# Optimization experiments

Measured on AMD Instinct MI355X. Metric: run time of the kernel, lower is better.

The kernel has to match this reference:

```python
import jax, jax.numpy as jnp
import numpy as np

EMBED_DIMS = [8, 16, 8]      # prod = 1024 = embed_dim
HIDDEN_DIMS = [16, 16, 16]   # prod = 4096 = hidden_dim
RANK = 16
B, S = 4, 1024


def _make_cores(key, in_dims, out_dims, rank):
    d = len(in_dims)
    ranks = [1] + [rank] * (d - 1) + [1]
    cores = []
    for k in range(d):
        key, sub = jax.random.split(key)
        shape = (ranks[k], in_dims[k], out_dims[k], ranks[k + 1])
        scale = 1.0 / np.sqrt(in_dims[k] * ranks[k])
        cores.append((scale * jax.random.normal(sub, shape, dtype=jnp.float32)))
    return cores


def setup_inputs() -> dict:
    key = jax.random.key(0)
    k_x, k1, k2, kb1, kb2 = jax.random.split(key, 5)
    x = jax.random.normal(k_x, (B, S, 1024), dtype=jnp.float32)
    fc1 = _make_cores(k1, EMBED_DIMS, HIDDEN_DIMS, RANK)
    fc2 = _make_cores(k2, HIDDEN_DIMS, EMBED_DIMS, RANK)
    b1 = 0.01 * jax.random.normal(kb1, (4096,), dtype=jnp.float32)
    b2 = 0.01 * jax.random.normal(kb2, (1024,), dtype=jnp.float32)
    return {
        "x": x,
        "fc1_c0": fc1[0], "fc1_c1": fc1[1], "fc1_c2": fc1[2], "fc1_b": b1,
        "fc2_c0": fc2[0], "fc2_c1": fc2[1], "fc2_c2": fc2[2], "fc2_b": b2,
    }


def tt_linear(x_flat, cores, bias, in_dims):
    """TT-matrix x batch-of-vectors product. x_flat: [N, prod(in_dims)].

    Cores: core_k has shape [r_{k-1}, n_k, m_k, r_k] with r_0 = r_d = 1.
    Invariant: acc is [r_{k-1}, n_k, rest] with rest laid out as
    (n_{k+1}..n_d, N, m_1..m_{k-1}).
    """
    N = x_flat.shape[0]
    acc = x_flat.reshape((N,) + tuple(in_dims))      # [N, n1..nd]
    acc = jnp.moveaxis(acc, 0, -1)                   # [n1..nd, N]
    acc = acc.reshape(in_dims[0], -1)[None]          # [1, n1, rest]
    d = len(cores)
    for k, c in enumerate(cores):
        # contract previous rank + current input mode
        acc = jnp.einsum('pnR,pnmq->Rmq', acc, c)    # [rest, m_k, r_k]
        if k < d - 1:
            n_next = in_dims[k + 1]
            R, m, q = acc.shape
            acc = acc.reshape(n_next, R // n_next, m, q)
            acc = jnp.transpose(acc, (3, 0, 1, 2)).reshape(q, n_next, -1)
    # final acc: [N * m1..m_{d-1}, m_d, 1] -> [N, M]
    return acc.reshape(N, -1) + bias


def reference(x, fc1_c0, fc1_c1, fc1_c2, fc1_b, fc2_c0, fc2_c1, fc2_c2, fc2_b):
    flat = x.reshape(-1, x.shape[-1])                        # [N, embed_dim]
    z1 = tt_linear(flat, [fc1_c0, fc1_c1, fc1_c2], fc1_b, EMBED_DIMS)   # [N, hidden]
    h1 = jax.nn.gelu(z1, approximate=False)                  # exact erf GELU (torch default)
    z2 = tt_linear(h1, [fc2_c0, fc2_c1, fc2_c2], fc2_b, HIDDEN_DIMS)    # [N, embed]
    return z2.reshape(*x.shape[:-1], z2.shape[-1])
```

## Files before the change

### kernel.cpp

```cpp
#include <hip/hip_runtime.h>
#include <stdint.h>

__device__ __forceinline__ float b2f(unsigned short u) {
    union { uint32_t i; float f; } v; v.i = ((uint32_t)u) << 16; return v.f;
}
__device__ __forceinline__ unsigned short f2b(float f) {
    union { float f; uint32_t i; } v; v.f = f;
    uint32_t r = v.i + 0x7fffu + ((v.i >> 16) & 1u);
    return (unsigned short)(r >> 16);
}

typedef __bf16 bf16x8 __attribute__((ext_vector_type(8)));
typedef float  f32x16 __attribute__((ext_vector_type(16)));

template<int N3, int M3>
__device__ __forceinline__ void build_T_body(int e,
                                             const float* __restrict__ c1,
                                             const float* __restrict__ c2,
                                             float* __restrict__ T) {
    int m3 = e % M3;
    int t  = e / M3;
    int n3 = t % N3;
    int rm = t / N3;
    float s = 0.f;
#pragma unroll
    for (int r2 = 0; r2 < 16; ++r2)
        s += c1[rm * 16 + r2] * c2[(r2 * N3 + n3) * M3 + m3];
    T[e] = s;
}

__global__ __launch_bounds__(256)
void prep_stage1(const float* __restrict__ c11, const float* __restrict__ c12,
                 float* __restrict__ T1,
                 const float* __restrict__ c21, const float* __restrict__ c22,
                 float* __restrict__ T2,
                 const float* __restrict__ x, unsigned short* __restrict__ xb) {
    const int b = blockIdx.x;
    if (b < 2048) {
        build_T_body<8, 16>(b * 256 + threadIdx.x, c11, c12, T1);
    } else if (b < 4096) {
        build_T_body<16, 8>((b - 2048) * 256 + threadIdx.x, c21, c22, T2);
    } else {
        const int t = (b - 4096) * 256 + threadIdx.x;
        const float4* p = (const float4*)(x + (size_t)t * 8);
        float4 f0 = p[0], f1 = p[1];
        int4 o;
        o.x = (uint32_t)f2b(f0.x) | ((uint32_t)f2b(f0.y) << 16);
        o.y = (uint32_t)f2b(f0.z) | ((uint32_t)f2b(f0.w) << 16);
        o.z = (uint32_t)f2b(f1.x) | ((uint32_t)f2b(f1.y) << 16);
        o.w = (uint32_t)f2b(f1.z) | ((uint32_t)f2b(f1.w) << 16);
        ((int4*)xb)[t] = o;
    }
}

template<int N1, int N2, int N3, int M1, int M2, int M3>
__device__ __forceinline__ void build_W_body(int t,
                                             const float* __restrict__ c0,
                                             const float* __restrict__ T,
                                             unsigned short* __restrict__ W) {
    constexpr int K = N1 * N2 * N3;
    int m3 = t % M3;
    int m2 = (t / M3) % M2;
    int n2 = (t / (M3 * M2)) % N2;
    int m1 = (t / (M3 * M2 * N2)) % M1;
    int n1 =  t / (M3 * M2 * N2 * M1);

    float c0r[16];
    const float4* c0p = (const float4*)(c0 + (n1 * M1 + m1) * 16);
#pragma unroll
    for (int i = 0; i < 4; ++i) ((float4*)c0r)[i] = c0p[i];

    float acc[N3] = {};
#pragma unroll
    for (int r1 = 0; r1 < 16; ++r1) {
        const float* Tp = T + (size_t)(((r1 * 16 + n2) * 16 + m2) * N3) * M3 + m3;
#pragma unroll
        for (int n3 = 0; n3 < N3; ++n3)
            acc[n3] += c0r[r1] * Tp[n3 * M3];
    }

    unsigned short ob[N3];
#pragma unroll
    for (int n3 = 0; n3 < N3; ++n3) ob[n3] = f2b(acc[n3]);

    unsigned short* dst = W + (size_t)((m1 * M2 + m2) * M3 + m3) * K
                            + (n1 * N2 + n2) * N3;
#pragma unroll
    for (int c = 0; c < N3 / 8; ++c)
        ((int4*)dst)[c] = ((const int4*)ob)[c];
}

__global__ __launch_bounds__(256)
void build_W_both(const float* __restrict__ c10, const float* __restrict__ T1,
                  unsigned short* __restrict__ W1,
                  const float* __restrict__ c20, const float* __restrict__ T2,
                  unsigned short* __restrict__ W2) {
    const int b = blockIdx.x;
    if (b < 2048)
        build_W_body<8, 16, 8, 16, 16, 16>(b * 256 + threadIdx.x, c10, T1, W1);
    else
        build_W_body<16, 16, 16, 8, 16, 8>((b - 2048) * 256 + threadIdx.x, c20, T2, W2);
}

template<int N1, int N2, int N3, int M1, int M2, int M3>
__global__ __launch_bounds__(256)
void build_W(const float* __restrict__ c0, const float* __restrict__ T,
             unsigned short* __restrict__ W) {
    build_W_body<N1, N2, N3, M1, M2, M3>(blockIdx.x * 256 + threadIdx.x, c0, T, W);
}

template<int BM, int BN, int KTOT, int GX, bool DO_GELU, bool C_F32>
__global__ __launch_bounds__(256, 2)
void gemm_gl(const unsigned short* __restrict__ A,
             const unsigned short* __restrict__ Bt,
             const float* __restrict__ bias,
             void* __restrict__ Cv,
             int Ncols)
{
    constexpr int BK   = 64;
    constexpr int NT   = KTOT / BK;
    constexpr int ASZ  = BM * BK;
    constexpr int BSZ  = BN * BK;
    constexpr int BUFE = ASZ + BSZ;
    constexpr int ACH  = BM / 32;
    constexpr int BCH  = BN / 32;
    constexpr int FI   = BM / 64, FJ = BN / 64;

    extern __shared__ unsigned short sh[];

    const int tid   = threadIdx.x;
    const int lane  = tid & 63;
    const int wave  = tid >> 6;
    const int m32   = lane & 31;
    const int khalf = lane >> 5;
    const int waveM = (wave >> 1) * (BM / 2);
    const int waveN = (wave & 1) * (BN / 2);
    const int srow  = tid >> 3;
    const int sslot = tid & 7;

    int lin = (int)blockIdx.y * GX + (int)blockIdx.x;
    const int total = GX * (int)gridDim.y;
    lin = (lin & 7) * (total >> 3) + (lin >> 3);
    const int rowBase = (lin / GX) * BM;
    const int colBase = (lin % GX) * BN;

#define GL_STAGE(B_, K0_)                                                     \
    {                                                                         \
        _Pragma("unroll")                                                     \
        for (int c = 0; c < ACH; ++c) {                                       \
            const int r  = c * 32 + srow;                                     \
            const int jg = sslot ^ (r & 7) ^ ((r >> 3) & 7);                  \
            const unsigned short* src = A +                                   \
                (size_t)(rowBase + r) * KTOT + (K0_) + jg * 8;                \
            unsigned short* dst = sh + (B_) * BUFE + c * 2048 + wave * 512;   \
            __builtin_amdgcn_global_load_lds(                                 \
                (const __attribute__((address_space(1))) void*)src,           \
                (__attribute__((address_space(3))) void*)dst, 16, 0, 0);      \
        }                                                                     \
        _Pragma("unroll")                                                     \
        for (int c = 0; c < BCH; ++c) {                                       \
            const int r  = c * 32 + srow;                                     \
            const int jg = sslot ^ (r & 7) ^ ((r >> 3) & 7);                  \
            const unsigned short* src = Bt +                                  \
                (size_t)(colBase + r) * KTOT + (K0_) + jg * 8;                \
            unsigned short* dst = sh + (B_) * BUFE + ASZ + c * 2048           \
                                  + wave * 512;                               \
            __builtin_amdgcn_global_load_lds(                                 \
                (const __attribute__((address_space(1))) void*)src,           \
                (__attribute__((address_space(3))) void*)dst, 16, 0, 0);      \
        }                                                                     \
    }

    f32x16 acc[FI][FJ] = {};

    GL_STAGE(0, 0)
    __syncthreads();

    int buf = 0;
    for (int t = 0; t < NT; ++t) {
        if (t + 1 < NT) GL_STAGE(buf ^ 1, (t + 1) * BK)

        const unsigned short* Ab = sh + buf * BUFE;
        const unsigned short* Bb = Ab + ASZ;
#pragma unroll
        for (int ks = 0; ks < 4; ++ks) {
            bf16x8 a_f[FI], b_f[FJ];
            const int g = ks * 2 + khalf;
#pragma unroll
            for (int i = 0; i < FI; ++i) {
                const int r = waveM + i * 32 + m32;
                const int key = (r & 7) ^ ((r >> 3) & 7);
                a_f[i] = *(const bf16x8*)&Ab[r * BK + ((g ^ key) << 3)];
            }
#pragma unroll
            for (int j = 0; j < FJ; ++j) {
                const int r = waveN + j * 32 + m32;
                const int key = (r & 7) ^ ((r >> 3) & 7);
                b_f[j] = *(const bf16x8*)&Bb[r * BK + ((g ^ key) << 3)];
            }
#pragma unroll
            for (int i = 0; i < FI; ++i)
#pragma unroll
                for (int j = 0; j < FJ; ++j)
                    acc[i][j] = __builtin_amdgcn_mfma_f32_32x32x16_bf16(
                        a_f[i], b_f[j], acc[i][j], 0, 0, 0);
        }
        __syncthreads();
        buf ^= 1;
    }
#undef GL_STAGE

#pragma unroll
    for (int i = 0; i < FI; ++i) {
#pragma unroll
        for (int j = 0; j < FJ; ++j) {
            const int col = colBase + waveN + j * 32 + m32;
            const float bv = bias[col];
#pragma unroll
            for (int reg = 0; reg < 16; ++reg) {
                const int row = rowBase + waveM + i * 32 +
                                (reg & 3) + 8 * (reg >> 2) + 4 * khalf;
                float z = acc[i][j][reg] + bv;
                if (DO_GELU)
                    z = 0.5f * z * (1.f + erff(z * 0.70710678118654752f));
                const size_t off = (size_t)row * Ncols + col;
                if (C_F32) ((float*)Cv)[off] = z;
                else       ((unsigned short*)Cv)[off] = f2b(z);
            }
        }
    }
}

#define PC_COMPUTE(BUF)                                                       \
    {                                                                         \
        _Pragma("unroll")                                                     \
        for (int ks = 0; ks < 4; ++ks) {                                      \
            bf16x8 a_f[FI], b_f[FJ];                                          \
            _Pragma("unroll")                                                 \
            for (int i = 0; i < FI; ++i) {                                    \
                const int key = (m32 & 7) ^                                   \
                    (((waveM >> 3) + 4 * i + (m32 >> 3)) & 7);                \
                const int slot = ((ks * 2 + khalf) ^ key) * 8;                \
                a_f[i] = *(const bf16x8*)&As[(BUF) * ASZ +                    \
                          (waveM + i * 32 + m32) * BK + slot];                \
            }                                                                 \
            _Pragma("unroll")                                                 \
            for (int j = 0; j < FJ; ++j) {                                    \
                const int key = (m32 & 7) ^                                   \
                    (((waveN >> 3) + 4 * j + (m32 >> 3)) & 7);                \
                const int slot = ((ks * 2 + khalf) ^ key) * 8;                \
                b_f[j] = *(const bf16x8*)&Bs[(BUF) * BSZ +                    \
                          (waveN + j * 32 + m32) * BK + slot];                \
            }                                                                 \
            _Pragma("unroll")                                                 \
            for (int i = 0; i < FI; ++i)                                      \
                _Pragma("unroll")                                             \
                for (int j = 0; j < FJ; ++j)                                  \
                    acc[i][j] = __builtin_amdgcn_mfma_f32_32x32x16_bf16(      \
                        a_f[i], b_f[j], acc[i][j], 0, 0, 0);                  \
        }                                                                     \
    }

template<int BM, int BN, int KTOT, bool DO_GELU, bool A_F32, bool C_F32>
__global__ __launch_bounds__(512, 4)
void gemm_pc(const void* __restrict__ Av,
             const unsigned short* __restrict__ Bt,
             const float* __restrict__ bias,
             void* __restrict__ Cv,
             int Ncols) {
    constexpr int BK  = 64;
    constexpr int CA  = BM / 8;
    constexpr int CB  = BN / 8;
    constexpr int PA  = CA / 4;
    constexpr int PB  = CB / 4;
    constexpr int FI  = BM / 64;
    constexpr int FJ  = BN / 64;
    constexpr int ASZ = BM * BK;
    constexpr int BSZ = BN * BK;
    __shared__ unsigned short As[2 * ASZ];
    __shared__ unsigned short Bs[2 * BSZ];

    const int tid  = threadIdx.x;
    const int lane = tid & 63;
    const int wave = tid >> 6;
    const int rowBase = blockIdx.y * BM;
    const int colBase = blockIdx.x * BN;

    const int lr    = lane >> 3;
    const int jj    = lane & 7;
    const int m32   = lane & 31;
    const int khalf = lane >> 5;

    if (wave >= 4) {
        const int pw = wave - 4;
#pragma unroll
        for (int it = 0; it < PA; ++it) {
            const int c  = pw * PA + it;
            const int jg = jj ^ lr ^ (c & 7);
            const size_t aoff = (size_t)(rowBase + c * 8 + lr) * KTOT + jg * 8;
            int4 v;
            if (A_F32) {
                const float* ga = (const float*)Av + aoff;
                float4 f0 = *(const float4*)ga;
                float4 f1 = *(const float4*)(ga + 4);
                v.x = (uint32_t)f2b(f0.x) | ((uint32_t)f2b(f0.y) << 16);
                v.y = (uint32_t)f2b(f0.z) | ((uint32_t)f2b(f0.w) << 16);
                v.z = (uint32_t)f2b(f1.x) | ((uint32_t)f2b(f1.y) << 16);
                v.w = (uint32_t)f2b(f1.z) | ((uint32_t)f2b(f1.w) << 16);
            } else {
                v = *(const int4*)((const unsigned short*)Av + aoff);
            }
            *(int4*)&As[c * 512 + lane * 8] = v;
        }
#pragma unroll
        for (int it = 0; it < PB; ++it) {
            const int c  = pw * PB + it;
            const int jg = jj ^ lr ^ (c & 7);
            *(int4*)&Bs[c * 512 + lane * 8] =
                *(const int4*)(Bt + (size_t)(colBase + c * 8 + lr) * KTOT + jg * 8);
        }
        __syncthreads();

        int buf = 1;
        for (int k0 = BK; k0 < KTOT; k0 += BK) {
            int4 aR[PA], bR[PB];
#pragma unroll
            for (int it = 0; it < PA; ++it) {
                const int c  = pw * PA + it;
                const int jg = jj ^ lr ^ (c & 7);
                const size_t aoff = (size_t)(rowBase + c * 8 + lr) * KTOT + k0 + jg * 8;
                if (A_F32) {
                    const float* ga = (const float*)Av + aoff;
                    float4 f0 = *(const float4*)ga;
                    float4 f1 = *(const float4*)(ga + 4);
                    int4 v;
                    v.x = (uint32_t)f2b(f0.x) | ((uint32_t)f2b(f0.y) << 16);
                    v.y = (uint32_t)f2b(f0.z) | ((uint32_t)f2b(f0.w) << 16);
                    v.z = (uint32_t)f2b(f1.x) | ((uint32_t)f2b(f1.y) << 16);
                    v.w = (uint32_t)f2b(f1.z) | ((uint32_t)f2b(f1.w) << 16);
                    aR[it] = v;
                } else {
                    aR[it] = *(const int4*)((const unsigned short*)Av + aoff);
                }
            }
#pragma unroll
            for (int it = 0; it < PB; ++it) {
                const int c  = pw * PB + it;
                const int jg = jj ^ lr ^ (c & 7);
                bR[it] = *(const int4*)(Bt + (size_t)(colBase + c * 8 + lr) * KTOT + k0 + jg * 8);
            }
#pragma unroll
            for (int it = 0; it < PA; ++it) {
                const int c = pw * PA + it;
                *(int4*)&As[buf * ASZ + c * 512 + lane * 8] = aR[it];
            }
#pragma unroll
            for (int it = 0; it < PB; ++it) {
                const int c = pw * PB + it;
                *(int4*)&Bs[buf * BSZ + c * 512 + lane * 8] = bR[it];
            }
            __syncthreads();
            buf ^= 1;
        }
    } else {
        const int waveM = (wave >> 1) * (BM / 2);
        const int waveN = (wave & 1) * (BN / 2);
        f32x16 acc[FI][FJ] = {};

        __syncthreads();

        int cur = 0;
        for (int k0 = BK; k0 < KTOT; k0 += BK) {
            PC_COMPUTE(cur)
            __syncthreads();
            cur ^= 1;
        }
        PC_COMPUTE(cur)

#pragma unroll
        for (int i = 0; i < FI; ++i) {
#pragma unroll
            for (int j = 0; j < FJ; ++j) {
                const int col = colBase + waveN + j * 32 + m32;
                const float bv = bias[col];
#pragma unroll
                for (int reg = 0; reg < 16; ++reg) {
                    const int row = rowBase + waveM + i * 32 +
                                    (reg & 3) + 8 * (reg >> 2) + 4 * khalf;
                    float z = acc[i][j][reg] + bv;
                    if (DO_GELU)
                        z = 0.5f * z * (1.f + erff(z * 0.70710678118654752f));
                    const size_t off = (size_t)row * Ncols + col;
                    if (C_F32) ((float*)Cv)[off] = z;
                    else       ((unsigned short*)Cv)[off] = f2b(z);
                }
            }
        }
    }
}

extern "C" void kernel_launch(void* const* d_in, const int* in_sizes, int n_in,
                              void* d_out, int out_size, void* d_ws, size_t ws_size,
                              hipStream_t stream) {
    const float* x      = (const float*)d_in[0];
    const float* fc1_c0 = (const float*)d_in[1];
    const float* fc1_c1 = (const float*)d_in[2];
    const float* fc1_c2 = (const float*)d_in[3];
    const float* fc1_b  = (const float*)d_in[4];
    const float* fc2_c0 = (const float*)d_in[5];
    const float* fc2_c1 = (const float*)d_in[6];
    const float* fc2_c2 = (const float*)d_in[7];
    const float* fc2_b  = (const float*)d_in[8];

    float* T1 = (float*)d_out;
    float* T2 = (float*)d_out + 524288;
    unsigned short* xb = (unsigned short*)((char*)d_out + (4u << 20));

    char* ws = (char*)d_ws;
    const bool big = ws_size >= (48ull << 20);

    constexpr int LDS1 = 2 * (128 + 128) * 64 * 2;
    constexpr int LDS2 = 2 * (128 + 64) * 64 * 2;
    static bool attr_done = false;
    if (!attr_done) {
        attr_done = true;
        (void)hipFuncSetAttribute(
            reinterpret_cast<const void*>(
                &gemm_gl<128, 128, 1024, 32, true, false>),
            hipFuncAttributeMaxDynamicSharedMemorySize, LDS1);
        (void)hipFuncSetAttribute(
            reinterpret_cast<const void*>(
                &gemm_gl<128, 64, 4096, 16, false, true>),
            hipFuncAttributeMaxDynamicSharedMemorySize, LDS2);
    }

    prep_stage1<<<6144, 256, 0, stream>>>(fc1_c1, fc1_c2, T1,
                                          fc2_c1, fc2_c2, T2, x, xb);

    if (big) {
        unsigned short* W1 = (unsigned short*)ws;
        unsigned short* W2 = (unsigned short*)(ws + (8u << 20));
        unsigned short* h  = (unsigned short*)(ws + (16u << 20));

        build_W_both<<<3072, 256, 0, stream>>>(fc1_c0, T1, W1,
                                               fc2_c0, T2, W2);
        gemm_gl<128, 128, 1024, 32, true, false>
            <<<dim3(32, 32), 256, LDS1, stream>>>(xb, W1, fc1_b, h, 4096);
        gemm_gl<128, 64, 4096, 16, false, true>
            <<<dim3(16, 32), 256, LDS2, stream>>>(h, W2, fc2_b, d_out, 1024);
    } else {
        unsigned short* W = (unsigned short*)ws;
        unsigned short* h = (unsigned short*)(ws + (8u << 20));

        build_W<8, 16, 8, 16, 16, 16><<<2048, 256, 0, stream>>>(fc1_c0, T1, W);
        gemm_pc<128, 128, 1024, true, false, false>
            <<<dim3(32, 32), 512, 0, stream>>>(xb, W, fc1_b, h, 4096);
        build_W<16, 16, 16, 8, 16, 8><<<1024, 256, 0, stream>>>(fc2_c0, T2, W);
        gemm_pc<128, 64, 4096, false, false, true>
            <<<dim3(16, 32), 512, 0, stream>>>(h, W, fc2_b, d_out, 1024);
    }
}
```

Measured before the change: 219.2 us.

## Use split-K with atomic accumulation for second GEMM and shrink K tile

Replaces the GEMM kernel with a variant that uses a 32-wide K tile, a smaller LDS footprint and a 4-blocks-per-CU launch bound. The second GEMM is split into two K chunks across a z grid dimension, and partial sums are added with atomics into an output that a separate kernel pre-fills with the bias. The aim is more blocks in flight and better occupancy for the tall-K second GEMM. The cost is an extra bias-fill launch, atomic traffic, and non-deterministic float summation order.

```diff
diff --git a/kernel.cpp b/kernel.cpp
--- a/kernel.cpp
+++ b/kernel.cpp
@@ -109,21 +109,28 @@
     build_W_body<N1, N2, N3, M1, M2, M3>(blockIdx.x * 256 + threadIdx.x, c0, T, W);
 }
 
-template<int BM, int BN, int KTOT, int GX, bool DO_GELU, bool C_F32>
-__global__ __launch_bounds__(256, 2)
-void gemm_gl(const unsigned short* __restrict__ A,
-             const unsigned short* __restrict__ Bt,
-             const float* __restrict__ bias,
-             void* __restrict__ Cv,
-             int Ncols)
+__global__ __launch_bounds__(256)
+void bias_fill(const float* __restrict__ b, float4* __restrict__ out) {
+    int t = blockIdx.x * 256 + threadIdx.x;
+    out[t] = ((const float4*)b)[t & 255];
+}
+
+template<int BM, int BN, int KCH, int KSTR, int GX, int GY,
+         bool DO_GELU, bool ATOMIC>
+__global__ __launch_bounds__(256, 4)
+void gemm_gl2(const unsigned short* __restrict__ A,
+              const unsigned short* __restrict__ Bt,
+              const float* __restrict__ bias,
+              void* __restrict__ Cv,
+              int Ncols)
 {
-    constexpr int BK   = 64;
-    constexpr int NT   = KTOT / BK;
+    constexpr int BK   = 32;
+    constexpr int NT   = KCH / BK;
     constexpr int ASZ  = BM * BK;
     constexpr int BSZ  = BN * BK;
     constexpr int BUFE = ASZ + BSZ;
-    constexpr int ACH  = BM / 32;
-    constexpr int BCH  = BN / 32;
+    constexpr int ACH  = BM / 64;
+    constexpr int BCH  = BN / 64;
     constexpr int FI   = BM / 64, FJ = BN / 64;
 
     extern __shared__ unsigned short sh[];
@@ -135,23 +142,24 @@
     const int khalf = lane >> 5;
     const int waveM = (wave >> 1) * (BM / 2);
     const int waveN = (wave & 1) * (BN / 2);
-    const int srow  = tid >> 3;
-    const int sslot = tid & 7;
-
-    int lin = (int)blockIdx.y * GX + (int)blockIdx.x;
-    const int total = GX * (int)gridDim.y;
+    const int srow  = tid >> 2;
+    const int sslot = tid & 3;
+
+    int lin = ((int)blockIdx.z * GY + (int)blockIdx.y) * GX + (int)blockIdx.x;
+    const int total = GX * GY * (int)gridDim.z;
     lin = (lin & 7) * (total >> 3) + (lin >> 3);
-    const int rowBase = (lin / GX) * BM;
     const int colBase = (lin % GX) * BN;
-
-#define GL_STAGE(B_, K0_)                                                     \
+    const int rowBase = ((lin / GX) % GY) * BM;
+    const int kOff    = (lin / (GX * GY)) * KCH;
+
+#define GL2_STAGE(B_, K0_)                                                    \
     {                                                                         \
         _Pragma("unroll")                                                     \
         for (int c = 0; c < ACH; ++c) {                                       \
-            const int r  = c * 32 + srow;                                     \
-            const int jg = sslot ^ (r & 7) ^ ((r >> 3) & 7);                  \
+            const int r  = c * 64 + srow;                                     \
+            const int jg = sslot ^ (((r >> 1) & 3) ^ ((r >> 3) & 3));         \
             const unsigned short* src = A +                                   \
-                (size_t)(rowBase + r) * KTOT + (K0_) + jg * 8;                \
+                (size_t)(rowBase + r) * KSTR + (K0_) + jg * 8;                \
             unsigned short* dst = sh + (B_) * BUFE + c * 2048 + wave * 512;   \
             __builtin_amdgcn_global_load_lds(                                 \
                 (const __attribute__((address_space(1))) void*)src,           \
@@ -159,10 +167,10 @@
         }                                                                     \
         _Pragma("unroll")                                                     \
         for (int c = 0; c < BCH; ++c) {                                       \
-            const int r  = c * 32 + srow;                                     \
-            const int jg = sslot ^ (r & 7) ^ ((r >> 3) & 7);                  \
+            const int r  = c * 64 + srow;                                     \
+            const int jg = sslot ^ (((r >> 1) & 3) ^ ((r >> 3) & 3));         \
             const unsigned short* src = Bt +                                  \
-                (size_t)(colBase + r) * KTOT + (K0_) + jg * 8;                \
+                (size_t)(colBase + r) * KSTR + (K0_) + jg * 8;                \
             unsigned short* dst = sh + (B_) * BUFE + ASZ + c * 2048           \
                                   + wave * 512;                               \
             __builtin_amdgcn_global_load_lds(                                 \
@@ -173,29 +181,29 @@
 
     f32x16 acc[FI][FJ] = {};
 
-    GL_STAGE(0, 0)
+    GL2_STAGE(0, kOff)
     __syncthreads();
 
     int buf = 0;
     for (int t = 0; t < NT; ++t) {
-        if (t + 1 < NT) GL_STAGE(buf ^ 1, (t + 1) * BK)
+        if (t + 1 < NT) GL2_STAGE(buf ^ 1, kOff + (t + 1) * BK)
 
         const unsigned short* Ab = sh + buf * BUFE;
         const unsigned short* Bb = Ab + ASZ;
 #pragma unroll
-        for (int ks = 0; ks < 4; ++ks) {
+        for (int ks = 0; ks < 2; ++ks) {
             bf16x8 a_f[FI], b_f[FJ];
             const int g = ks * 2 + khalf;
 #pragma unroll
             for (int i = 0; i < FI; ++i) {
                 const int r = waveM + i * 32 + m32;
-                const int key = (r & 7) ^ ((r >> 3) & 7);
+                const int key = ((r >> 1) & 3) ^ ((r >> 3) & 3);
                 a_f[i] = *(const bf16x8*)&Ab[r * BK + ((g ^ key) << 3)];
             }
 #pragma unroll
             for (int j = 0; j < FJ; ++j) {
                 const int r = waveN + j * 32 + m32;
-                const int key = (r & 7) ^ ((r >> 3) & 7);
+                const int key = ((r >> 1) & 3) ^ ((r >> 3) & 3);
                 b_f[j] = *(const bf16x8*)&Bb[r * BK + ((g ^ key) << 3)];
             }
 #pragma unroll
@@ -208,24 +216,27 @@
         __syncthreads();
         buf ^= 1;
     }
-#undef GL_STAGE
+#undef GL2_STAGE
 
 #pragma unroll
     for (int i = 0; i < FI; ++i) {
 #pragma unroll
         for (int j = 0; j < FJ; ++j) {
             const int col = colBase + waveN + j * 32 + m32;
-            const float bv = bias[col];
+            const float bv = ATOMIC ? 0.f : bias[col];
 #pragma unroll
             for (int reg = 0; reg < 16; ++reg) {
                 const int row = rowBase + waveM + i * 32 +
                                 (reg & 3) + 8 * (reg >> 2) + 4 * khalf;
-                float z = acc[i][j][reg] + bv;
-                if (DO_GELU)
-                    z = 0.5f * z * (1.f + erff(z * 0.70710678118654752f));
                 const size_t off = (size_t)row * Ncols + col;
-                if (C_F32) ((float*)Cv)[off] = z;
-                else       ((unsigned short*)Cv)[off] = f2b(z);
+                if (ATOMIC) {
+                    unsafeAtomicAdd((float*)Cv + off, acc[i][j][reg]);
+                } else {
+                    float z = acc[i][j][reg] + bv;
+                    if (DO_GELU)
+                        z = 0.5f * z * (1.f + erff(z * 0.70710678118654752f));
+                    ((unsigned short*)Cv)[off] = f2b(z);
+                }
             }
         }
     }
@@ -419,20 +430,7 @@
     char* ws = (char*)d_ws;
     const bool big = ws_size >= (48ull << 20);
 
-    constexpr int LDS1 = 2 * (128 + 128) * 64 * 2;
-    constexpr int LDS2 = 2 * (128 + 64) * 64 * 2;
-    static bool attr_done = false;
-    if (!attr_done) {
-        attr_done = true;
-        (void)hipFuncSetAttribute(
-            reinterpret_cast<const void*>(
-                &gemm_gl<128, 128, 1024, 32, true, false>),
-            hipFuncAttributeMaxDynamicSharedMemorySize, LDS1);
-        (void)hipFuncSetAttribute(
-            reinterpret_cast<const void*>(
-                &gemm_gl<128, 64, 4096, 16, false, true>),
-            hipFuncAttributeMaxDynamicSharedMemorySize, LDS2);
-    }
+    constexpr int DLDS = 40 << 10;
 
     prep_stage1<<<6144, 256, 0, stream>>>(fc1_c1, fc1_c2, T1,
                                           fc2_c1, fc2_c2, T2, x, xb);
@@ -444,10 +442,11 @@
 
         build_W_both<<<3072, 256, 0, stream>>>(fc1_c0, T1, W1,
                                                fc2_c0, T2, W2);
-        gemm_gl<128, 128, 1024, 32, true, false>
-            <<<dim3(32, 32), 256, LDS1, stream>>>(xb, W1, fc1_b, h, 4096);
-        gemm_gl<128, 64, 4096, 16, false, true>
-            <<<dim3(16, 32), 256, LDS2, stream>>>(h, W2, fc2_b, d_out, 1024);
+        gemm_gl2<128, 128, 1024, 1024, 32, 32, true, false>
+            <<<dim3(32, 32, 1), 256, DLDS, stream>>>(xb, W1, fc1_b, h, 4096);
+        bias_fill<<<4096, 256, 0, stream>>>(fc2_b, (float4*)d_out);
+        gemm_gl2<128, 64, 2048, 4096, 16, 32, false, true>
+            <<<dim3(16, 32, 2), 256, DLDS, stream>>>(h, W2, fc2_b, d_out, 1024);
     } else {
         unsigned short* W = (unsigned short*)ws;
         unsigned short* h = (unsigned short*)(ws + (8u << 20));
```

Result: slower. 248.8 us (+13.5%).
